# Performance work log

Hardware: AMD Instinct MI355X
Metric: run time of the kernel (lower is better)

Reference implementation:

```python
import jax, jax.numpy as jnp
import numpy as np

N = 100000      # nodes
E = 1600000     # edges (self-loops added in reference, as PyG GATConv does)
DIN = 512
DOUT = 16
H = 8           # heads (both layers)
C1 = 8          # out_channels of gat1
NEG_SLOPE = 0.2


def setup_inputs() -> dict:
    key = jax.random.key(0)
    ks = jax.random.split(key, 12)
    s = 0.05  # small init scale
    return {
        "x": jax.random.normal(ks[0], (N, DIN), jnp.float32),
        "edge_index": jax.random.randint(ks[1], (2, E), 0, N, jnp.int32),
        "W1": jax.random.normal(ks[2], (DIN, H * C1), jnp.float32) * s,
        "att_src1": jax.random.normal(ks[3], (H, C1), jnp.float32) * s,
        "att_dst1": jax.random.normal(ks[4], (H, C1), jnp.float32) * s,
        "bias1": jnp.zeros((H * C1,), jnp.float32),
        "prelu_w": jnp.float32(0.25),
        "W2": jax.random.normal(ks[5], (H * C1, H * DOUT), jnp.float32) * s,
        "att_src2": jax.random.normal(ks[6], (H, DOUT), jnp.float32) * s,
        "att_dst2": jax.random.normal(ks[7], (H, DOUT), jnp.float32) * s,
        "bias2": jnp.zeros((DOUT,), jnp.float32),
    }


def gat_layer(x, src, dst, W, a_src, a_dst, bias, heads, outc, concat):
    """PyG-style GATConv (eval mode, self-loops already in src/dst)."""
    n = x.shape[0]
    h = (x @ W).reshape(n, heads, outc)                 # [N, H, C]
    alpha_s = jnp.sum(h * a_src, axis=-1)               # [N, H]
    alpha_d = jnp.sum(h * a_dst, axis=-1)               # [N, H]
    # per-edge score, softmax grouped by destination node
    e = jax.nn.leaky_relu(alpha_s[src] + alpha_d[dst], NEG_SLOPE)   # [E', H]
    emax = jax.ops.segment_max(e, dst, num_segments=n)              # [N, H]
    ex = jnp.exp(e - emax[dst])
    denom = jax.ops.segment_sum(ex, dst, num_segments=n)            # [N, H]
    alpha = ex / denom[dst]                                         # [E', H]
    # weighted aggregation of source features
    out = jax.ops.segment_sum(h[src] * alpha[..., None], dst, num_segments=n)  # [N, H, C]
    out = out.reshape(n, heads * outc) if concat else out.mean(axis=1)
    return out + bias


def reference(x, edge_index, W1, att_src1, att_dst1, bias1, prelu_w,
              W2, att_src2, att_dst2, bias2):
    # add self-loops (PyG GATConv default add_self_loops=True)
    loops = jnp.arange(N, dtype=edge_index.dtype)
    src = jnp.concatenate([edge_index[0], loops])
    dst = jnp.concatenate([edge_index[1], loops])

    h = gat_layer(x, src, dst, W1, att_src1, att_dst1, bias1, H, C1, True)   # [N, 64]
    h = jnp.where(h >= 0, h, prelu_w * h)                                    # PReLU
    h = gat_layer(h, src, dst, W2, att_src2, att_dst2, bias2, H, DOUT, False)  # [N, DOUT]
    return jax.nn.log_softmax(h, axis=1)
```

## Files before the change

### kernel.cpp

```cpp
#include <hip/hip_runtime.h>
#include <hip/hip_bf16.h>

#define NN 100000
#define EE 1600000
#define ET (EE + NN)
#define NBK 391
#define NBLK 208
#define STAGE_CAP 5120

typedef unsigned short ushort_t;
typedef short short8 __attribute__((ext_vector_type(8)));
typedef float f32x4 __attribute__((ext_vector_type(4)));

static __device__ __forceinline__ float b2f(unsigned short u) {
    return __uint_as_float(((unsigned int)u) << 16);
}
static __device__ __forceinline__ unsigned short f2b(float f) {
    unsigned int x = __float_as_uint(f);
    return (unsigned short)((x + 0x7fffu + ((x >> 16) & 1u)) >> 16);
}

__global__ __launch_bounds__(256) void ktrans(const float* __restrict__ W1,
                                              const float* __restrict__ W2,
                                              ushort_t* __restrict__ W1T,
                                              ushort_t* __restrict__ W2T) {
    int tid = blockIdx.x * 256 + threadIdx.x;
    if (tid < 32768) {
        int k = tid >> 6, c = tid & 63;
        W1T[c * 512 + k] = f2b(W1[tid]);
    } else if (tid < 40960) {
        int t = tid - 32768;
        int k = t >> 7, c = t & 127;
        W2T[c * 64 + k] = f2b(W2[t]);
    }
}

__global__ __launch_bounds__(256) void kgemm1(const float* __restrict__ x,
                                              const ushort_t* __restrict__ w1t,
                                              ushort_t* __restrict__ h1) {
    __shared__ __align__(16) ushort_t xs[64][136];
    const int tid = threadIdx.x;
    const int wid = tid >> 6, lane = tid & 63;
    const int l15 = lane & 15, qq = lane >> 4;
    const int row0 = blockIdx.x * 64;
    f32x4 acc[4];
#pragma unroll
    for (int i = 0; i < 4; ++i) acc[i] = (f32x4)0.f;
    for (int kc = 0; kc < 4; ++kc) {
        float4 f[8];
#pragma unroll
        for (int i = 0; i < 8; ++i) {
            int f4i = tid + 256 * i;
            int rr = f4i >> 5;
            int cc = f4i & 31;
            long gr = (long)min(row0 + rr, NN - 1);
            f[i] = *(const float4*)(x + gr * 512 + kc * 128 + cc * 4);
        }
        __syncthreads();
#pragma unroll
        for (int i = 0; i < 8; ++i) {
            int f4i = tid + 256 * i;
            int rr = f4i >> 5, cc = f4i & 31;
            uint2 uu;
            uu.x = ((unsigned)f2b(f[i].y) << 16) | f2b(f[i].x);
            uu.y = ((unsigned)f2b(f[i].w) << 16) | f2b(f[i].z);
            *(uint2*)&xs[rr][cc * 4] = uu;
        }
        __syncthreads();
#pragma unroll
        for (int ks = 0; ks < 4; ++ks) {
            short8 b = *(const short8*)(w1t + (size_t)(wid * 16 + l15) * 512 + kc * 128 + ks * 32 + qq * 8);
#pragma unroll
            for (int mt = 0; mt < 4; ++mt) {
                short8 a = *(const short8*)&xs[mt * 16 + l15][ks * 32 + qq * 8];
                acc[mt] = __builtin_amdgcn_mfma_f32_16x16x32_bf16(a, b, acc[mt], 0, 0, 0);
            }
        }
    }
#pragma unroll
    for (int mt = 0; mt < 4; ++mt) {
        int node = row0 + mt * 16 + qq * 4;
#pragma unroll
        for (int rr = 0; rr < 4; ++rr) {
            if (node + rr < NN)
                h1[(size_t)(node + rr) * 64 + wid * 16 + l15] = f2b(acc[mt][rr]);
        }
    }
}

__global__ __launch_bounds__(256) void kgemm2(const ushort_t* __restrict__ hin,
                                              const ushort_t* __restrict__ w2t,
                                              ushort_t* __restrict__ h2) {
    __shared__ __align__(16) ushort_t xs[64][72];
    const int tid = threadIdx.x;
    const int wid = tid >> 6, lane = tid & 63;
    const int l15 = lane & 15, qq = lane >> 4;
    const int row0 = blockIdx.x * 64;
    const int r = tid >> 2, seg = tid & 3;
    const long grow = (long)min(row0 + r, NN - 1);
    const uint4* gp = (const uint4*)(hin + grow * 64 + seg * 16);
    uint4 v0 = gp[0], v1 = gp[1];
    uint4* lp = (uint4*)&xs[r][seg * 16];
    lp[0] = v0; lp[1] = v1;
    __syncthreads();
    f32x4 acc[4][2];
#pragma unroll
    for (int i = 0; i < 4; ++i)
#pragma unroll
        for (int j = 0; j < 2; ++j) acc[i][j] = (f32x4)0.f;
#pragma unroll
    for (int ks = 0; ks < 2; ++ks) {
        short8 a[4];
#pragma unroll
        for (int mt = 0; mt < 4; ++mt)
            a[mt] = *(const short8*)&xs[mt * 16 + l15][ks * 32 + qq * 8];
#pragma unroll
        for (int nt = 0; nt < 2; ++nt) {
            short8 b = *(const short8*)(w2t + (size_t)(wid * 32 + nt * 16 + l15) * 64 + ks * 32 + qq * 8);
#pragma unroll
            for (int mt = 0; mt < 4; ++mt)
                acc[mt][nt] = __builtin_amdgcn_mfma_f32_16x16x32_bf16(a[mt], b, acc[mt][nt], 0, 0, 0);
        }
    }
#pragma unroll
    for (int mt = 0; mt < 4; ++mt) {
        int node = row0 + mt * 16 + qq * 4;
#pragma unroll
        for (int nt = 0; nt < 2; ++nt) {
            int col = wid * 32 + nt * 16 + l15;
#pragma unroll
            for (int rr = 0; rr < 4; ++rr) {
                if (node + rr < NN)
                    h2[(size_t)(node + rr) * 128 + col] = f2b(acc[mt][nt][rr]);
            }
        }
    }
}


__global__ __launch_bounds__(256) void kbinh(const int* __restrict__ ei,
                                             int* __restrict__ bbcnt) {
    __shared__ int hist[NBK];
    const int t = threadIdx.x, blk = blockIdx.x;
    for (int i = t; i < NBK; i += 256) hist[i] = 0;
    __syncthreads();
    const int e0 = blk * 8192;
#pragma unroll
    for (int i = 0; i < 32; ++i) {
        int e = e0 + t + 256 * i;
        if (e < ET) {
            int dst = (e < EE) ? ei[EE + e] : (e - EE);
            atomicAdd(&hist[dst >> 8], 1);
        }
    }
    __syncthreads();
    for (int i = t; i < NBK; i += 256) bbcnt[blk * NBK + i] = hist[i];
}

__global__ __launch_bounds__(512) void kbscan(int* __restrict__ bbcnt,
                                              int* __restrict__ bbase) {
    __shared__ int tot[512];
    const int t = threadIdx.x;
    int total = 0;
    if (t < NBK) {
        int run = 0;
#pragma unroll 4
        for (int blk = 0; blk < NBLK; ++blk) {
            int idx = blk * NBK + t;
            int v = bbcnt[idx];
            bbcnt[idx] = run;
            run += v;
        }
        total = run;
    }
    tot[t] = total;
    __syncthreads();
    for (int off = 1; off < 512; off <<= 1) {
        int u = (t >= off) ? tot[t - off] : 0;
        __syncthreads();
        tot[t] += u;
        __syncthreads();
    }
    if (t < NBK) bbase[t] = tot[t] - total;
    if (t == 0) bbase[NBK] = ET;
}

__global__ __launch_bounds__(256) void kbinsct(const int* __restrict__ ei,
                                               const int* __restrict__ bbcnt,
                                               const int* __restrict__ bbase,
                                               unsigned* __restrict__ pairs) {
    __shared__ int cur[NBK];
    const int t = threadIdx.x, blk = blockIdx.x;
    for (int i = t; i < NBK; i += 256) cur[i] = bbase[i] + bbcnt[blk * NBK + i];
    __syncthreads();
    const int e0 = blk * 8192;
#pragma unroll
    for (int i = 0; i < 32; ++i) {
        int e = e0 + t + 256 * i;
        if (e < ET) {
            int src, dst;
            if (e < EE) { src = ei[e]; dst = ei[EE + e]; } else { src = dst = e - EE; }
            int pos = atomicAdd(&cur[dst >> 8], 1);
            pairs[pos] = (unsigned)src | ((unsigned)(dst & 255) << 17);
        }
    }
}

__global__ __launch_bounds__(256) void kscat2(const int* __restrict__ bbase,
                                              const unsigned* __restrict__ pairs,
                                              int* __restrict__ rowp,
                                              int* __restrict__ srt) {
    __shared__ int hist[256];
    __shared__ int scn[256];
    __shared__ int cur[256];
    __shared__ unsigned stage[STAGE_CAP];
    const int t = threadIdx.x, b = blockIdx.x;
    const int j0 = bbase[b], j1 = bbase[b + 1];
    const int cnt = j1 - j0;
    hist[t] = 0;
    __syncthreads();
    for (int i = t; i < cnt; i += 256) {
        unsigned p = pairs[j0 + i];
        if (i < STAGE_CAP) stage[i] = p;
        atomicAdd(&hist[p >> 17], 1);
    }
    __syncthreads();
    const int h = hist[t];
    scn[t] = h;
    __syncthreads();
    for (int off = 1; off < 256; off <<= 1) {
        int u = (t >= off) ? scn[t - off] : 0;
        __syncthreads();
        scn[t] += u;
        __syncthreads();
    }
    const int pref = scn[t] - h;
    const int node = b * 256 + t;
    if (node < NN) rowp[node] = j0 + pref;
    if (b == 0 && t == 0) rowp[NN] = ET;
    cur[t] = pref;
    __syncthreads();
    for (int i = t; i < cnt; i += 256) {
        unsigned p = (i < STAGE_CAP) ? stage[i] : pairs[j0 + i];
        int l = (int)(p >> 17);
        int pos = atomicAdd(&cur[l], 1);
        srt[j0 + pos] = (int)(p & 0x1FFFFu);
    }
}

__global__ __launch_bounds__(256) void kagg1(const int* __restrict__ rowp,
                                             const int* __restrict__ srt,
                                             const ushort_t* __restrict__ h1,
                                             const float* __restrict__ aws,
                                             const float* __restrict__ awd,
                                             const float* __restrict__ b1,
                                             const float* __restrict__ pw,
                                             ushort_t* __restrict__ hin) {
    int tid = blockIdx.x * 256 + threadIdx.x;
    int n = tid >> 4;
    int sub = tid & 15;
    int h = sub >> 1, half = sub & 1;
    float as_w[8], ad_w[8];
#pragma unroll
    for (int c = 0; c < 8; ++c) { as_w[c] = aws[h * 8 + c]; ad_w[c] = awd[h * 8 + c]; }
    uint4 hd = *(const uint4*)(h1 + (size_t)n * 64 + h * 8);
    const ushort_t* hdp = (const ushort_t*)&hd;
    float ad = 0.f;
#pragma unroll
    for (int c = 0; c < 8; ++c) ad += b2f(hdp[c]) * ad_w[c];
    int j0 = rowp[n], j1 = rowp[n + 1];
    float num[8]; float den = 0.f;
#pragma unroll
    for (int c = 0; c < 8; ++c) num[c] = 0.f;
    int j = j0 + half;
    uint4 hv;
    if (j < j1) {
        int s = srt[j];
        hv = *(const uint4*)(h1 + (size_t)s * 64 + h * 8);
    }
    while (j < j1) {
        int jn = j + 2;
        uint4 hn;
        if (jn < j1) {
            int sn = srt[jn];
            hn = *(const uint4*)(h1 + (size_t)sn * 64 + h * 8);
        }
        const ushort_t* hp = (const ushort_t*)&hv;
        float va[8];
#pragma unroll
        for (int c = 0; c < 8; ++c) va[c] = b2f(hp[c]);
        float sc = ad;
#pragma unroll
        for (int c = 0; c < 8; ++c) sc += va[c] * as_w[c];
        sc = (sc >= 0.f) ? sc : 0.2f * sc;
        float w = __expf(sc);
        den += w;
#pragma unroll
        for (int c = 0; c < 8; ++c) num[c] += w * va[c];
        j = jn;
        hv = hn;
    }
#pragma unroll
    for (int c = 0; c < 8; ++c) num[c] += __shfl_xor(num[c], 1);
    den += __shfl_xor(den, 1);
    if (half == 0) {
        float inv = 1.f / den;
        float pwf = pw[0];
        ushort_t o[8];
#pragma unroll
        for (int c = 0; c < 8; ++c) {
            float v = num[c] * inv + b1[h * 8 + c];
            v = (v >= 0.f) ? v : pwf * v;
            o[c] = f2b(v);
        }
        *(uint4*)(hin + (size_t)n * 64 + h * 8) = *(uint4*)o;
    }
}

__global__ __launch_bounds__(256) void kagg2(const int* __restrict__ rowp,
                                             const int* __restrict__ srt,
                                             const ushort_t* __restrict__ h2,
                                             const float* __restrict__ aws,
                                             const float* __restrict__ awd,
                                             const float* __restrict__ b2,
                                             float* __restrict__ out) {
    __shared__ float red[16][17];
    int t = threadIdx.x;
    int nl = t >> 4, sub = t & 15;
    int h = sub >> 1, half = sub & 1;
    int n = blockIdx.x * 16 + nl;
    for (int i = t; i < 16 * 17; i += 256) ((float*)red)[i] = 0.f;
    __syncthreads();
    float as_w[16], ad_w[16];
#pragma unroll
    for (int c = 0; c < 16; ++c) { as_w[c] = aws[h * 16 + c]; ad_w[c] = awd[h * 16 + c]; }
    uint4 d0 = *(const uint4*)(h2 + (size_t)n * 128 + h * 16);
    uint4 d1 = *(const uint4*)(h2 + (size_t)n * 128 + h * 16 + 8);
    const ushort_t* dp0 = (const ushort_t*)&d0;
    const ushort_t* dp1 = (const ushort_t*)&d1;
    float ad = 0.f;
#pragma unroll
    for (int c = 0; c < 8; ++c) { ad += b2f(dp0[c]) * ad_w[c]; ad += b2f(dp1[c]) * ad_w[8 + c]; }
    int j0 = rowp[n], j1 = rowp[n + 1];
    float num[16]; float den = 0.f;
#pragma unroll
    for (int c = 0; c < 16; ++c) num[c] = 0.f;
    int j = j0 + half;
    uint4 v0, v1;
    if (j < j1) {
        int s = srt[j];
        const uint4* rp = (const uint4*)(h2 + (size_t)s * 128 + h * 16);
        v0 = rp[0]; v1 = rp[1];
    }
    while (j < j1) {
        int jn = j + 2;
        uint4 n0, n1;
        if (jn < j1) {
            int sn = srt[jn];
            const uint4* rp = (const uint4*)(h2 + (size_t)sn * 128 + h * 16);
            n0 = rp[0]; n1 = rp[1];
        }
        const ushort_t* p0 = (const ushort_t*)&v0;
        const ushort_t* p1 = (const ushort_t*)&v1;
        float va[16];
#pragma unroll
        for (int c = 0; c < 8; ++c) { va[c] = b2f(p0[c]); va[8 + c] = b2f(p1[c]); }
        float sc = ad;
#pragma unroll
        for (int c = 0; c < 16; ++c) sc += va[c] * as_w[c];
        sc = (sc >= 0.f) ? sc : 0.2f * sc;
        float w = __expf(sc);
        den += w;
#pragma unroll
        for (int c = 0; c < 16; ++c) num[c] += w * va[c];
        j = jn;
        v0 = n0; v1 = n1;
    }
#pragma unroll
    for (int c = 0; c < 16; ++c) num[c] += __shfl_xor(num[c], 1);
    den += __shfl_xor(den, 1);
    float sden = 0.125f / den;
#pragma unroll
    for (int k = 0; k < 8; ++k) {
        int c = half * 8 + ((h + k) & 7);
        atomicAdd(&red[nl][c], num[c] * sden);
    }
    __syncthreads();
    if (t < 16) {
        float v[16];
#pragma unroll
        for (int d = 0; d < 16; ++d) v[d] = red[t][d] + b2[d];
        float m = v[0];
#pragma unroll
        for (int d = 1; d < 16; ++d) m = fmaxf(m, v[d]);
        float sum = 0.f;
#pragma unroll
        for (int d = 0; d < 16; ++d) sum += __expf(v[d] - m);
        float ls = __logf(sum) + m;
        float* op = out + (size_t)(blockIdx.x * 16 + t) * 16;
#pragma unroll
        for (int d = 0; d < 16; ++d) op[d] = v[d] - ls;
    }
}

extern "C" void kernel_launch(void* const* d_in, const int* in_sizes, int n_in,
                              void* d_out, int out_size, void* d_ws, size_t ws_size,
                              hipStream_t stream) {
    const float* x    = (const float*)d_in[0];
    const int*   ei   = (const int*)d_in[1];
    const float* W1   = (const float*)d_in[2];
    const float* aws1 = (const float*)d_in[3];
    const float* awd1 = (const float*)d_in[4];
    const float* b1   = (const float*)d_in[5];
    const float* pw   = (const float*)d_in[6];
    const float* W2   = (const float*)d_in[7];
    const float* aws2 = (const float*)d_in[8];
    const float* awd2 = (const float*)d_in[9];
    const float* b2   = (const float*)d_in[10];
    float* out = (float*)d_out;

    char* ws = (char*)d_ws;
    int*      srt   = (int*)(ws + 0);
    int*      rowp  = (int*)(ws + 6800000);
    int*      bbcnt = (int*)(ws + 7200256);
    int*      bbase = (int*)(ws + 7600384);
    unsigned* pairs = (unsigned*)(ws + 8000000);
    ushort_t* hin   = (ushort_t*)(ws + 8000000);
    ushort_t* h1    = (ushort_t*)(ws + 20800000);
    ushort_t* h2    = (ushort_t*)(ws + 20800000);
    ushort_t* W1T   = (ushort_t*)(ws + 46400000);
    ushort_t* W2T   = (ushort_t*)(ws + 46465536);

    ktrans<<<160, 256, 0, stream>>>(W1, W2, W1T, W2T);
    kgemm1<<<1563, 256, 0, stream>>>(x, W1T, h1);
    kbinh<<<NBLK, 256, 0, stream>>>(ei, bbcnt);
    kbscan<<<1, 512, 0, stream>>>(bbcnt, bbase);
    kbinsct<<<NBLK, 256, 0, stream>>>(ei, bbcnt, bbase, pairs);
    kscat2<<<NBK, 256, 0, stream>>>(bbase, pairs, rowp, srt);
    kagg1<<<6250, 256, 0, stream>>>(rowp, srt, h1, aws1, awd1, b1, pw, hin);
    kgemm2<<<1563, 256, 0, stream>>>(hin, W2T, h2);
    kagg2<<<6250, 256, 0, stream>>>(rowp, srt, h2, aws2, awd2, b2, out);
}
```

Baseline: 575.4 us.

## Co-schedule CSR build with GEMM1 and precompute per-node attention scores

Merges the weight transpose with the destination histogram and splits the first GEMM across the two CSR scatter kernels. Independent work now shares launches and can fill idle CUs during the small scatter grids. Adds kalpha1/kalpha2 kernels that compute per-node source and destination attention logits once, so the aggregation loops read a scalar per edge instead of recomputing a dot product per edge. Shrinks the staging buffer so the fused kernel's shared memory stays smaller. The cost is extra launches, extra global traffic for the logit arrays, and a scattered 4-byte load per edge.

```diff
diff --git a/kernel.cpp b/kernel.cpp
--- a/kernel.cpp
+++ b/kernel.cpp
@@ -6,7 +6,7 @@
 #define ET (EE + NN)
 #define NBK 391
 #define NBLK 208
-#define STAGE_CAP 5120
+#define STAGE_CAP 4096
 
 typedef unsigned short ushort_t;
 typedef short short8 __attribute__((ext_vector_type(8)));
@@ -20,29 +20,13 @@
     return (unsigned short)((x + 0x7fffu + ((x >> 16) & 1u)) >> 16);
 }
 
-__global__ __launch_bounds__(256) void ktrans(const float* __restrict__ W1,
-                                              const float* __restrict__ W2,
-                                              ushort_t* __restrict__ W1T,
-                                              ushort_t* __restrict__ W2T) {
-    int tid = blockIdx.x * 256 + threadIdx.x;
-    if (tid < 32768) {
-        int k = tid >> 6, c = tid & 63;
-        W1T[c * 512 + k] = f2b(W1[tid]);
-    } else if (tid < 40960) {
-        int t = tid - 32768;
-        int k = t >> 7, c = t & 127;
-        W2T[c * 64 + k] = f2b(W2[t]);
-    }
-}
-
-__global__ __launch_bounds__(256) void kgemm1(const float* __restrict__ x,
-                                              const ushort_t* __restrict__ w1t,
-                                              ushort_t* __restrict__ h1) {
-    __shared__ __align__(16) ushort_t xs[64][136];
-    const int tid = threadIdx.x;
+static __device__ void gemm1_body(const float* __restrict__ x,
+                                  const ushort_t* __restrict__ w1t,
+                                  ushort_t* __restrict__ h1,
+                                  char* smem_, int row0, int tid) {
+    ushort_t (*xs)[136] = (ushort_t (*)[136])smem_;
     const int wid = tid >> 6, lane = tid & 63;
     const int l15 = lane & 15, qq = lane >> 4;
-    const int row0 = blockIdx.x * 64;
     f32x4 acc[4];
 #pragma unroll
     for (int i = 0; i < 4; ++i) acc[i] = (f32x4)0.f;
@@ -85,6 +69,255 @@
             if (node + rr < NN)
                 h1[(size_t)(node + rr) * 64 + wid * 16 + l15] = f2b(acc[mt][rr]);
         }
+    }
+}
+
+__global__ __launch_bounds__(256) void kfuse0(const float* __restrict__ W1,
+                                              const float* __restrict__ W2,
+                                              ushort_t* __restrict__ W1T,
+                                              ushort_t* __restrict__ W2T,
+                                              const int* __restrict__ ei,
+                                              int* __restrict__ bbcnt) {
+    __shared__ int hist[NBK];
+    const int t = threadIdx.x;
+    if ((int)blockIdx.x < 160) {
+        int tid = blockIdx.x * 256 + t;
+        if (tid < 32768) {
+            int k = tid >> 6, c = tid & 63;
+            W1T[c * 512 + k] = f2b(W1[tid]);
+        } else if (tid < 40960) {
+            int q = tid - 32768;
+            int k = q >> 7, c = q & 127;
+            W2T[c * 64 + k] = f2b(W2[q]);
+        }
+    } else {
+        const int blk = blockIdx.x - 160;
+        for (int i = t; i < NBK; i += 256) hist[i] = 0;
+        __syncthreads();
+        const int e0 = blk * 8192;
+#pragma unroll
+        for (int i = 0; i < 32; ++i) {
+            int e = e0 + t + 256 * i;
+            if (e < ET) {
+                int dst = (e < EE) ? ei[EE + e] : (e - EE);
+                atomicAdd(&hist[dst >> 8], 1);
+            }
+        }
+        __syncthreads();
+        for (int i = t; i < NBK; i += 256) bbcnt[blk * NBK + i] = hist[i];
+    }
+}
+
+__global__ __launch_bounds__(512) void kbscan(int* __restrict__ bbcnt,
+                                              int* __restrict__ bbase) {
+    __shared__ int tot[512];
+    const int t = threadIdx.x;
+    int total = 0;
+    if (t < NBK) {
+        int run = 0;
+#pragma unroll 8
+        for (int blk = 0; blk < NBLK; ++blk) {
+            int idx = blk * NBK + t;
+            int v = bbcnt[idx];
+            bbcnt[idx] = run;
+            run += v;
+        }
+        total = run;
+    }
+    tot[t] = total;
+    __syncthreads();
+    for (int off = 1; off < 512; off <<= 1) {
+        int u = (t >= off) ? tot[t - off] : 0;
+        __syncthreads();
+        tot[t] += u;
+        __syncthreads();
+    }
+    if (t < NBK) bbase[t] = tot[t] - total;
+    if (t == 0) bbase[NBK] = ET;
+}
+
+__global__ __launch_bounds__(256) void kfuse1(const int* __restrict__ ei,
+                                              const int* __restrict__ bbcnt,
+                                              const int* __restrict__ bbase,
+                                              unsigned* __restrict__ pairs,
+                                              const float* __restrict__ x,
+                                              const ushort_t* __restrict__ w1t,
+                                              ushort_t* __restrict__ h1) {
+    __shared__ __align__(16) char smem[17408];
+    const int t = threadIdx.x;
+    if ((int)blockIdx.x < NBLK) {
+        int* cur = (int*)smem;
+        const int blk = blockIdx.x;
+        for (int i = t; i < NBK; i += 256) cur[i] = bbase[i] + bbcnt[blk * NBK + i];
+        __syncthreads();
+        const int e0 = blk * 8192;
+#pragma unroll
+        for (int i = 0; i < 32; ++i) {
+            int e = e0 + t + 256 * i;
+            if (e < ET) {
+                int src, dst;
+                if (e < EE) { src = ei[e]; dst = ei[EE + e]; } else { src = dst = e - EE; }
+                int pos = atomicAdd(&cur[dst >> 8], 1);
+                pairs[pos] = (unsigned)src | ((unsigned)(dst & 255) << 17);
+            }
+        }
+    } else {
+        gemm1_body(x, w1t, h1, smem, (blockIdx.x - NBLK) * 64, t);
+    }
+}
+
+__global__ __launch_bounds__(256) void kfuse2(const int* __restrict__ bbase,
+                                              const unsigned* __restrict__ pairs,
+                                              int* __restrict__ rowp,
+                                              int* __restrict__ srt,
+                                              const float* __restrict__ x,
+                                              const ushort_t* __restrict__ w1t,
+                                              ushort_t* __restrict__ h1) {
+    __shared__ __align__(16) char smem[19456];
+    const int t = threadIdx.x;
+    if ((int)blockIdx.x < NBK) {
+        int* hist = (int*)smem;
+        int* scn = hist + 256;
+        int* cur = scn + 256;
+        unsigned* stage = (unsigned*)(smem + 3072);
+        const int b = blockIdx.x;
+        const int j0 = bbase[b], j1 = bbase[b + 1];
+        const int cnt = j1 - j0;
+        hist[t] = 0;
+        __syncthreads();
+        for (int i = t; i < cnt; i += 256) {
+            unsigned p = pairs[j0 + i];
+            if (i < STAGE_CAP) stage[i] = p;
+            atomicAdd(&hist[p >> 17], 1);
+        }
+        __syncthreads();
+        const int h = hist[t];
+        scn[t] = h;
+        __syncthreads();
+        for (int off = 1; off < 256; off <<= 1) {
+            int u = (t >= off) ? scn[t - off] : 0;
+            __syncthreads();
+            scn[t] += u;
+            __syncthreads();
+        }
+        const int pref = scn[t] - h;
+        const int node = b * 256 + t;
+        if (node < NN) rowp[node] = j0 + pref;
+        if (b == 0 && t == 0) rowp[NN] = ET;
+        cur[t] = pref;
+        __syncthreads();
+        for (int i = t; i < cnt; i += 256) {
+            unsigned p = (i < STAGE_CAP) ? stage[i] : pairs[j0 + i];
+            int l = (int)(p >> 17);
+            int pos = atomicAdd(&cur[l], 1);
+            srt[j0 + pos] = (int)(p & 0x1FFFFu);
+        }
+    } else {
+        gemm1_body(x, w1t, h1, smem, (782 + (int)blockIdx.x - NBK) * 64, t);
+    }
+}
+
+__global__ __launch_bounds__(256) void kalpha1(const ushort_t* __restrict__ h1,
+                                               const float* __restrict__ aws,
+                                               const float* __restrict__ awd,
+                                               float* __restrict__ a1s,
+                                               float* __restrict__ a1d) {
+    int tid = blockIdx.x * 256 + threadIdx.x;
+    int n = tid >> 3, h = tid & 7;
+    uint4 v = *(const uint4*)(h1 + (size_t)n * 64 + h * 8);
+    const ushort_t* p = (const ushort_t*)&v;
+    float s = 0.f, d = 0.f;
+#pragma unroll
+    for (int c = 0; c < 8; ++c) {
+        float f = b2f(p[c]);
+        s += f * aws[h * 8 + c];
+        d += f * awd[h * 8 + c];
+    }
+    a1s[tid] = s;
+    a1d[tid] = d;
+}
+
+__global__ __launch_bounds__(256) void kalpha2(const ushort_t* __restrict__ h2,
+                                               const float* __restrict__ aws,
+                                               const float* __restrict__ awd,
+                                               float* __restrict__ a2s,
+                                               float* __restrict__ a2d) {
+    int tid = blockIdx.x * 256 + threadIdx.x;
+    int n = tid >> 3, h = tid & 7;
+    uint4 v0 = *(const uint4*)(h2 + (size_t)n * 128 + h * 16);
+    uint4 v1 = *(const uint4*)(h2 + (size_t)n * 128 + h * 16 + 8);
+    const ushort_t* p0 = (const ushort_t*)&v0;
+    const ushort_t* p1 = (const ushort_t*)&v1;
+    float s = 0.f, d = 0.f;
+#pragma unroll
+    for (int c = 0; c < 8; ++c) {
+        float fa = b2f(p0[c]), fb = b2f(p1[c]);
+        s += fa * aws[h * 16 + c];
+        d += fa * awd[h * 16 + c];
+        s += fb * aws[h * 16 + 8 + c];
+        d += fb * awd[h * 16 + 8 + c];
+    }
+    a2s[tid] = s;
+    a2d[tid] = d;
+}
+
+__global__ __launch_bounds__(256) void kagg1(const int* __restrict__ rowp,
+                                             const int* __restrict__ srt,
+                                             const ushort_t* __restrict__ h1,
+                                             const float* __restrict__ a1s,
+                                             const float* __restrict__ a1d,
+                                             const float* __restrict__ b1,
+                                             const float* __restrict__ pw,
+                                             ushort_t* __restrict__ hin) {
+    int tid = blockIdx.x * 256 + threadIdx.x;
+    int n = tid >> 4;
+    int sub = tid & 15;
+    int h = sub >> 1, half = sub & 1;
+    float ad = a1d[n * 8 + h];
+    int j0 = rowp[n], j1 = rowp[n + 1];
+    float num[8]; float den = 0.f;
+#pragma unroll
+    for (int c = 0; c < 8; ++c) num[c] = 0.f;
+    int j = j0 + half;
+    uint4 hv; float al = 0.f;
+    if (j < j1) {
+        int s = srt[j];
+        al = a1s[s * 8 + h];
+        hv = *(const uint4*)(h1 + (size_t)s * 64 + h * 8);
+    }
+    while (j < j1) {
+        int jn = j + 2;
+        uint4 hn; float aln = 0.f;
+        if (jn < j1) {
+            int sn = srt[jn];
+            aln = a1s[sn * 8 + h];
+            hn = *(const uint4*)(h1 + (size_t)sn * 64 + h * 8);
+        }
+        float sc = al + ad;
+        sc = (sc >= 0.f) ? sc : 0.2f * sc;
+        float w = __expf(sc);
+        den += w;
+        const ushort_t* hp = (const ushort_t*)&hv;
+#pragma unroll
+        for (int c = 0; c < 8; ++c) num[c] += w * b2f(hp[c]);
+        j = jn;
+        hv = hn;
+        al = aln;
+    }
+#pragma unroll
+    for (int c = 0; c < 8; ++c) num[c] += __shfl_xor(num[c], 1);
+    den += __shfl_xor(den, 1);
+    if (half == 0) {
+        float inv = 1.f / den;
+        float pwf = pw[0];
+        ushort_t o[8];
+#pragma unroll
+        for (int c = 0; c < 8; ++c) {
+            float v = num[c] * inv + b1[h * 8 + c];
+            v = (v >= 0.f) ? v : pwf * v;
+            o[c] = f2b(v);
+        }
+        *(uint4*)(hin + (size_t)n * 64 + h * 8) = *(uint4*)o;
     }
 }
 
@@ -137,191 +370,11 @@
     }
 }
 
-
-__global__ __launch_bounds__(256) void kbinh(const int* __restrict__ ei,
-                                             int* __restrict__ bbcnt) {
-    __shared__ int hist[NBK];
-    const int t = threadIdx.x, blk = blockIdx.x;
-    for (int i = t; i < NBK; i += 256) hist[i] = 0;
-    __syncthreads();
-    const int e0 = blk * 8192;
-#pragma unroll
-    for (int i = 0; i < 32; ++i) {
-        int e = e0 + t + 256 * i;
-        if (e < ET) {
-            int dst = (e < EE) ? ei[EE + e] : (e - EE);
-            atomicAdd(&hist[dst >> 8], 1);
-        }
-    }
-    __syncthreads();
-    for (int i = t; i < NBK; i += 256) bbcnt[blk * NBK + i] = hist[i];
-}
-
-__global__ __launch_bounds__(512) void kbscan(int* __restrict__ bbcnt,
-                                              int* __restrict__ bbase) {
-    __shared__ int tot[512];
-    const int t = threadIdx.x;
-    int total = 0;
-    if (t < NBK) {
-        int run = 0;
-#pragma unroll 4
-        for (int blk = 0; blk < NBLK; ++blk) {
-            int idx = blk * NBK + t;
-            int v = bbcnt[idx];
-            bbcnt[idx] = run;
-            run += v;
-        }
-        total = run;
-    }
-    tot[t] = total;
-    __syncthreads();
-    for (int off = 1; off < 512; off <<= 1) {
-        int u = (t >= off) ? tot[t - off] : 0;
-        __syncthreads();
-        tot[t] += u;
-        __syncthreads();
-    }
-    if (t < NBK) bbase[t] = tot[t] - total;
-    if (t == 0) bbase[NBK] = ET;
-}
-
-__global__ __launch_bounds__(256) void kbinsct(const int* __restrict__ ei,
-                                               const int* __restrict__ bbcnt,
-                                               const int* __restrict__ bbase,
-                                               unsigned* __restrict__ pairs) {
-    __shared__ int cur[NBK];
-    const int t = threadIdx.x, blk = blockIdx.x;
-    for (int i = t; i < NBK; i += 256) cur[i] = bbase[i] + bbcnt[blk * NBK + i];
-    __syncthreads();
-    const int e0 = blk * 8192;
-#pragma unroll
-    for (int i = 0; i < 32; ++i) {
-        int e = e0 + t + 256 * i;
-        if (e < ET) {
-            int src, dst;
-            if (e < EE) { src = ei[e]; dst = ei[EE + e]; } else { src = dst = e - EE; }
-            int pos = atomicAdd(&cur[dst >> 8], 1);
-            pairs[pos] = (unsigned)src | ((unsigned)(dst & 255) << 17);
-        }
-    }
-}
-
-__global__ __launch_bounds__(256) void kscat2(const int* __restrict__ bbase,
-                                              const unsigned* __restrict__ pairs,
-                                              int* __restrict__ rowp,
-                                              int* __restrict__ srt) {
-    __shared__ int hist[256];
-    __shared__ int scn[256];
-    __shared__ int cur[256];
-    __shared__ unsigned stage[STAGE_CAP];
-    const int t = threadIdx.x, b = blockIdx.x;
-    const int j0 = bbase[b], j1 = bbase[b + 1];
-    const int cnt = j1 - j0;
-    hist[t] = 0;
-    __syncthreads();
-    for (int i = t; i < cnt; i += 256) {
-        unsigned p = pairs[j0 + i];
-        if (i < STAGE_CAP) stage[i] = p;
-        atomicAdd(&hist[p >> 17], 1);
-    }
-    __syncthreads();
-    const int h = hist[t];
-    scn[t] = h;
-    __syncthreads();
-    for (int off = 1; off < 256; off <<= 1) {
-        int u = (t >= off) ? scn[t - off] : 0;
-        __syncthreads();
-        scn[t] += u;
-        __syncthreads();
-    }
-    const int pref = scn[t] - h;
-    const int node = b * 256 + t;
-    if (node < NN) rowp[node] = j0 + pref;
-    if (b == 0 && t == 0) rowp[NN] = ET;
-    cur[t] = pref;
-    __syncthreads();
-    for (int i = t; i < cnt; i += 256) {
-        unsigned p = (i < STAGE_CAP) ? stage[i] : pairs[j0 + i];
-        int l = (int)(p >> 17);
-        int pos = atomicAdd(&cur[l], 1);
-        srt[j0 + pos] = (int)(p & 0x1FFFFu);
-    }
-}
-
-__global__ __launch_bounds__(256) void kagg1(const int* __restrict__ rowp,
-                                             const int* __restrict__ srt,
-                                             const ushort_t* __restrict__ h1,
-                                             const float* __restrict__ aws,
-                                             const float* __restrict__ awd,
-                                             const float* __restrict__ b1,
-                                             const float* __restrict__ pw,
-                                             ushort_t* __restrict__ hin) {
-    int tid = blockIdx.x * 256 + threadIdx.x;
-    int n = tid >> 4;
-    int sub = tid & 15;
-    int h = sub >> 1, half = sub & 1;
-    float as_w[8], ad_w[8];
-#pragma unroll
-    for (int c = 0; c < 8; ++c) { as_w[c] = aws[h * 8 + c]; ad_w[c] = awd[h * 8 + c]; }
-    uint4 hd = *(const uint4*)(h1 + (size_t)n * 64 + h * 8);
-    const ushort_t* hdp = (const ushort_t*)&hd;
-    float ad = 0.f;
-#pragma unroll
-    for (int c = 0; c < 8; ++c) ad += b2f(hdp[c]) * ad_w[c];
-    int j0 = rowp[n], j1 = rowp[n + 1];
-    float num[8]; float den = 0.f;
-#pragma unroll
-    for (int c = 0; c < 8; ++c) num[c] = 0.f;
-    int j = j0 + half;
-    uint4 hv;
-    if (j < j1) {
-        int s = srt[j];
-        hv = *(const uint4*)(h1 + (size_t)s * 64 + h * 8);
-    }
-    while (j < j1) {
-        int jn = j + 2;
-        uint4 hn;
-        if (jn < j1) {
-            int sn = srt[jn];
-            hn = *(const uint4*)(h1 + (size_t)sn * 64 + h * 8);
-        }
-        const ushort_t* hp = (const ushort_t*)&hv;
-        float va[8];
-#pragma unroll
-        for (int c = 0; c < 8; ++c) va[c] = b2f(hp[c]);
-        float sc = ad;
-#pragma unroll
-        for (int c = 0; c < 8; ++c) sc += va[c] * as_w[c];
-        sc = (sc >= 0.f) ? sc : 0.2f * sc;
-        float w = __expf(sc);
-        den += w;
-#pragma unroll
-        for (int c = 0; c < 8; ++c) num[c] += w * va[c];
-        j = jn;
-        hv = hn;
-    }
-#pragma unroll
-    for (int c = 0; c < 8; ++c) num[c] += __shfl_xor(num[c], 1);
-    den += __shfl_xor(den, 1);
-    if (half == 0) {
-        float inv = 1.f / den;
-        float pwf = pw[0];
-        ushort_t o[8];
-#pragma unroll
-        for (int c = 0; c < 8; ++c) {
-            float v = num[c] * inv + b1[h * 8 + c];
-            v = (v >= 0.f) ? v : pwf * v;
-            o[c] = f2b(v);
-        }
-        *(uint4*)(hin + (size_t)n * 64 + h * 8) = *(uint4*)o;
-    }
-}
-
 __global__ __launch_bounds__(256) void kagg2(const int* __restrict__ rowp,
                                              const int* __restrict__ srt,
                                              const ushort_t* __restrict__ h2,
-                                             const float* __restrict__ aws,
-                                             const float* __restrict__ awd,
+                                             const float* __restrict__ a2s,
+                                             const float* __restrict__ a2d,
                                              const float* __restrict__ b2,
                                              float* __restrict__ out) {
     __shared__ float red[16][17];
@@ -331,50 +384,42 @@
     int n = blockIdx.x * 16 + nl;
     for (int i = t; i < 16 * 17; i += 256) ((float*)red)[i] = 0.f;
     __syncthreads();
-    float as_w[16], ad_w[16];
-#pragma unroll
-    for (int c = 0; c < 16; ++c) { as_w[c] = aws[h * 16 + c]; ad_w[c] = awd[h * 16 + c]; }
-    uint4 d0 = *(const uint4*)(h2 + (size_t)n * 128 + h * 16);
-    uint4 d1 = *(const uint4*)(h2 + (size_t)n * 128 + h * 16 + 8);
-    const ushort_t* dp0 = (const ushort_t*)&d0;
-    const ushort_t* dp1 = (const ushort_t*)&d1;
-    float ad = 0.f;
-#pragma unroll
-    for (int c = 0; c < 8; ++c) { ad += b2f(dp0[c]) * ad_w[c]; ad += b2f(dp1[c]) * ad_w[8 + c]; }
+    float ad = a2d[n * 8 + h];
     int j0 = rowp[n], j1 = rowp[n + 1];
     float num[16]; float den = 0.f;
 #pragma unroll
     for (int c = 0; c < 16; ++c) num[c] = 0.f;
     int j = j0 + half;
-    uint4 v0, v1;
+    uint4 v0, v1; float al = 0.f;
     if (j < j1) {
         int s = srt[j];
+        al = a2s[s * 8 + h];
         const uint4* rp = (const uint4*)(h2 + (size_t)s * 128 + h * 16);
         v0 = rp[0]; v1 = rp[1];
     }
     while (j < j1) {
         int jn = j + 2;
-        uint4 n0, n1;
+        uint4 n0, n1; float aln = 0.f;
         if (jn < j1) {
             int sn = srt[jn];
+            aln = a2s[sn * 8 + h];
             const uint4* rp = (const uint4*)(h2 + (size_t)sn * 128 + h * 16);
             n0 = rp[0]; n1 = rp[1];
         }
-        const ushort_t* p0 = (const ushort_t*)&v0;
-        const ushort_t* p1 = (const ushort_t*)&v1;
-        float va[16];
-#pragma unroll
-        for (int c = 0; c < 8; ++c) { va[c] = b2f(p0[c]); va[8 + c] = b2f(p1[c]); }
-        float sc = ad;
-#pragma unroll
-        for (int c = 0; c < 16; ++c) sc += va[c] * as_w[c];
+        float sc = al + ad;
         sc = (sc >= 0.f) ? sc : 0.2f * sc;
         float w = __expf(sc);
         den += w;
-#pragma unroll
-        for (int c = 0; c < 16; ++c) num[c] += w * va[c];
+        const ushort_t* p0 = (const ushort_t*)&v0;
+        const ushort_t* p1 = (const ushort_t*)&v1;
+#pragma unroll
+        for (int c = 0; c < 8; ++c) {
+            num[c] += w * b2f(p0[c]);
+            num[8 + c] += w * b2f(p1[c]);
+        }
         j = jn;
         v0 = n0; v1 = n1;
+        al = aln;
     }
 #pragma unroll
     for (int c = 0; c < 16; ++c) num[c] += __shfl_xor(num[c], 1);
@@ -426,18 +471,22 @@
     int*      bbase = (int*)(ws + 7600384);
     unsigned* pairs = (unsigned*)(ws + 8000000);
     ushort_t* hin   = (ushort_t*)(ws + 8000000);
+    float*    a2s   = (float*)(ws + 8000000);
+    float*    a2d   = (float*)(ws + 11200000);
     ushort_t* h1    = (ushort_t*)(ws + 20800000);
     ushort_t* h2    = (ushort_t*)(ws + 20800000);
+    float*    a1s   = (float*)(ws + 33600000);
+    float*    a1d   = (float*)(ws + 36800000);
     ushort_t* W1T   = (ushort_t*)(ws + 46400000);
     ushort_t* W2T   = (ushort_t*)(ws + 46465536);
 
-    ktrans<<<160, 256, 0, stream>>>(W1, W2, W1T, W2T);
-    kgemm1<<<1563, 256, 0, stream>>>(x, W1T, h1);
-    kbinh<<<NBLK, 256, 0, stream>>>(ei, bbcnt);
+    kfuse0<<<160 + NBLK, 256, 0, stream>>>(W1, W2, W1T, W2T, ei, bbcnt);
     kbscan<<<1, 512, 0, stream>>>(bbcnt, bbase);
-    kbinsct<<<NBLK, 256, 0, stream>>>(ei, bbcnt, bbase, pairs);
-    kscat2<<<NBK, 256, 0, stream>>>(bbase, pairs, rowp, srt);
-    kagg1<<<6250, 256, 0, stream>>>(rowp, srt, h1, aws1, awd1, b1, pw, hin);
+    kfuse1<<<NBLK + 782, 256, 0, stream>>>(ei, bbcnt, bbase, pairs, x, W1T, h1);
+    kfuse2<<<NBK + 781, 256, 0, stream>>>(bbase, pairs, rowp, srt, x, W1T, h1);
+    kalpha1<<<3125, 256, 0, stream>>>(h1, aws1, awd1, a1s, a1d);
+    kagg1<<<6250, 256, 0, stream>>>(rowp, srt, h1, a1s, a1d, b1, pw, hin);
     kgemm2<<<1563, 256, 0, stream>>>(hin, W2T, h2);
-    kagg2<<<6250, 256, 0, stream>>>(rowp, srt, h2, aws2, awd2, b2, out);
-}
+    kalpha2<<<3125, 256, 0, stream>>>(h2, aws2, awd2, a2s, a2d);
+    kagg2<<<6250, 256, 0, stream>>>(rowp, srt, h2, a2s, a2d, b2, out);
+}
```

Measured after the change: 582.8 us. About the same (+1.3%).

## Co-schedule GEMM1 blocks with CSR build kernels and shuffle-reduce layer-2 output

Applied to the files above, without the earlier changes.

Merges the weight transpose with the destination histogram into one launch. The first GEMM is split into two halves that run as extra blocks inside the bin-scatter and local-sort kernels, so the memory-bound CSR construction overlaps with matrix compute and the separate launches go away. The second aggregation kernel now reduces heads with warp shuffles instead of shared-memory atomics and a barrier, and every lane writes one output. The staging capacity is reduced so the shared buffer fits the fused kernel, which sends more of the large buckets through the global-memory fallback.

```diff
diff --git a/kernel.cpp b/kernel.cpp
--- a/kernel.cpp
+++ b/kernel.cpp
@@ -6,7 +6,7 @@
 #define ET (EE + NN)
 #define NBK 391
 #define NBLK 208
-#define STAGE_CAP 5120
+#define STAGE_CAP 4096
 
 typedef unsigned short ushort_t;
 typedef short short8 __attribute__((ext_vector_type(8)));
@@ -20,29 +20,13 @@
     return (unsigned short)((x + 0x7fffu + ((x >> 16) & 1u)) >> 16);
 }
 
-__global__ __launch_bounds__(256) void ktrans(const float* __restrict__ W1,
-                                              const float* __restrict__ W2,
-                                              ushort_t* __restrict__ W1T,
-                                              ushort_t* __restrict__ W2T) {
-    int tid = blockIdx.x * 256 + threadIdx.x;
-    if (tid < 32768) {
-        int k = tid >> 6, c = tid & 63;
-        W1T[c * 512 + k] = f2b(W1[tid]);
-    } else if (tid < 40960) {
-        int t = tid - 32768;
-        int k = t >> 7, c = t & 127;
-        W2T[c * 64 + k] = f2b(W2[t]);
-    }
-}
-
-__global__ __launch_bounds__(256) void kgemm1(const float* __restrict__ x,
-                                              const ushort_t* __restrict__ w1t,
-                                              ushort_t* __restrict__ h1) {
-    __shared__ __align__(16) ushort_t xs[64][136];
-    const int tid = threadIdx.x;
+static __device__ void gemm1_body(const float* __restrict__ x,
+                                  const ushort_t* __restrict__ w1t,
+                                  ushort_t* __restrict__ h1,
+                                  char* smem_, int row0, int tid) {
+    ushort_t (*xs)[136] = (ushort_t (*)[136])smem_;
     const int wid = tid >> 6, lane = tid & 63;
     const int l15 = lane & 15, qq = lane >> 4;
-    const int row0 = blockIdx.x * 64;
     f32x4 acc[4];
 #pragma unroll
     for (int i = 0; i < 4; ++i) acc[i] = (f32x4)0.f;
@@ -85,6 +69,220 @@
             if (node + rr < NN)
                 h1[(size_t)(node + rr) * 64 + wid * 16 + l15] = f2b(acc[mt][rr]);
         }
+    }
+}
+
+__global__ __launch_bounds__(256) void kfuse0(const float* __restrict__ W1,
+                                              const float* __restrict__ W2,
+                                              ushort_t* __restrict__ W1T,
+                                              ushort_t* __restrict__ W2T,
+                                              const int* __restrict__ ei,
+                                              int* __restrict__ bbcnt) {
+    __shared__ int hist[NBK];
+    const int t = threadIdx.x;
+    if ((int)blockIdx.x < 160) {
+        int tid = blockIdx.x * 256 + t;
+        if (tid < 32768) {
+            int k = tid >> 6, c = tid & 63;
+            W1T[c * 512 + k] = f2b(W1[tid]);
+        } else if (tid < 40960) {
+            int q = tid - 32768;
+            int k = q >> 7, c = q & 127;
+            W2T[c * 64 + k] = f2b(W2[q]);
+        }
+    } else {
+        const int blk = blockIdx.x - 160;
+        for (int i = t; i < NBK; i += 256) hist[i] = 0;
+        __syncthreads();
+        const int e0 = blk * 8192;
+#pragma unroll
+        for (int i = 0; i < 32; ++i) {
+            int e = e0 + t + 256 * i;
+            if (e < ET) {
+                int dst = (e < EE) ? ei[EE + e] : (e - EE);
+                atomicAdd(&hist[dst >> 8], 1);
+            }
+        }
+        __syncthreads();
+        for (int i = t; i < NBK; i += 256) bbcnt[blk * NBK + i] = hist[i];
+    }
+}
+
+__global__ __launch_bounds__(512) void kbscan(int* __restrict__ bbcnt,
+                                              int* __restrict__ bbase) {
+    __shared__ int tot[512];
+    const int t = threadIdx.x;
+    int total = 0;
+    if (t < NBK) {
+        int run = 0;
+#pragma unroll 8
+        for (int blk = 0; blk < NBLK; ++blk) {
+            int idx = blk * NBK + t;
+            int v = bbcnt[idx];
+            bbcnt[idx] = run;
+            run += v;
+        }
+        total = run;
+    }
+    tot[t] = total;
+    __syncthreads();
+    for (int off = 1; off < 512; off <<= 1) {
+        int u = (t >= off) ? tot[t - off] : 0;
+        __syncthreads();
+        tot[t] += u;
+        __syncthreads();
+    }
+    if (t < NBK) bbase[t] = tot[t] - total;
+    if (t == 0) bbase[NBK] = ET;
+}
+
+__global__ __launch_bounds__(256) void kfuse1(const int* __restrict__ ei,
+                                              const int* __restrict__ bbcnt,
+                                              const int* __restrict__ bbase,
+                                              unsigned* __restrict__ pairs,
+                                              const float* __restrict__ x,
+                                              const ushort_t* __restrict__ w1t,
+                                              ushort_t* __restrict__ h1) {
+    __shared__ __align__(16) char smem[17408];
+    const int t = threadIdx.x;
+    if ((int)blockIdx.x < NBLK) {
+        int* cur = (int*)smem;
+        const int blk = blockIdx.x;
+        for (int i = t; i < NBK; i += 256) cur[i] = bbase[i] + bbcnt[blk * NBK + i];
+        __syncthreads();
+        const int e0 = blk * 8192;
+#pragma unroll
+        for (int i = 0; i < 32; ++i) {
+            int e = e0 + t + 256 * i;
+            if (e < ET) {
+                int src, dst;
+                if (e < EE) { src = ei[e]; dst = ei[EE + e]; } else { src = dst = e - EE; }
+                int pos = atomicAdd(&cur[dst >> 8], 1);
+                pairs[pos] = (unsigned)src | ((unsigned)(dst & 255) << 17);
+            }
+        }
+    } else {
+        gemm1_body(x, w1t, h1, smem, (blockIdx.x - NBLK) * 64, t);
+    }
+}
+
+__global__ __launch_bounds__(256) void kfuse2(const int* __restrict__ bbase,
+                                              const unsigned* __restrict__ pairs,
+                                              int* __restrict__ rowp,
+                                              int* __restrict__ srt,
+                                              const float* __restrict__ x,
+                                              const ushort_t* __restrict__ w1t,
+                                              ushort_t* __restrict__ h1) {
+    __shared__ __align__(16) char smem[19456];
+    const int t = threadIdx.x;
+    if ((int)blockIdx.x < NBK) {
+        int* hist = (int*)smem;
+        int* scn = hist + 256;
+        int* cur = scn + 256;
+        unsigned* stage = (unsigned*)(smem + 3072);
+        const int b = blockIdx.x;
+        const int j0 = bbase[b], j1 = bbase[b + 1];
+        const int cnt = j1 - j0;
+        hist[t] = 0;
+        __syncthreads();
+        for (int i = t; i < cnt; i += 256) {
+            unsigned p = pairs[j0 + i];
+            if (i < STAGE_CAP) stage[i] = p;
+            atomicAdd(&hist[p >> 17], 1);
+        }
+        __syncthreads();
+        const int h = hist[t];
+        scn[t] = h;
+        __syncthreads();
+        for (int off = 1; off < 256; off <<= 1) {
+            int u = (t >= off) ? scn[t - off] : 0;
+            __syncthreads();
+            scn[t] += u;
+            __syncthreads();
+        }
+        const int pref = scn[t] - h;
+        const int node = b * 256 + t;
+        if (node < NN) rowp[node] = j0 + pref;
+        if (b == 0 && t == 0) rowp[NN] = ET;
+        cur[t] = pref;
+        __syncthreads();
+        for (int i = t; i < cnt; i += 256) {
+            unsigned p = (i < STAGE_CAP) ? stage[i] : pairs[j0 + i];
+            int l = (int)(p >> 17);
+            int pos = atomicAdd(&cur[l], 1);
+            srt[j0 + pos] = (int)(p & 0x1FFFFu);
+        }
+    } else {
+        gemm1_body(x, w1t, h1, smem, (782 + (int)blockIdx.x - NBK) * 64, t);
+    }
+}
+
+__global__ __launch_bounds__(256) void kagg1(const int* __restrict__ rowp,
+                                             const int* __restrict__ srt,
+                                             const ushort_t* __restrict__ h1,
+                                             const float* __restrict__ aws,
+                                             const float* __restrict__ awd,
+                                             const float* __restrict__ b1,
+                                             const float* __restrict__ pw,
+                                             ushort_t* __restrict__ hin) {
+    int tid = blockIdx.x * 256 + threadIdx.x;
+    int n = tid >> 4;
+    int sub = tid & 15;
+    int h = sub >> 1, half = sub & 1;
+    float as_w[8], ad_w[8];
+#pragma unroll
+    for (int c = 0; c < 8; ++c) { as_w[c] = aws[h * 8 + c]; ad_w[c] = awd[h * 8 + c]; }
+    uint4 hd = *(const uint4*)(h1 + (size_t)n * 64 + h * 8);
+    const ushort_t* hdp = (const ushort_t*)&hd;
+    float ad = 0.f;
+#pragma unroll
+    for (int c = 0; c < 8; ++c) ad += b2f(hdp[c]) * ad_w[c];
+    int j0 = rowp[n], j1 = rowp[n + 1];
+    float num[8]; float den = 0.f;
+#pragma unroll
+    for (int c = 0; c < 8; ++c) num[c] = 0.f;
+    int j = j0 + half;
+    uint4 hv;
+    if (j < j1) {
+        int s = srt[j];
+        hv = *(const uint4*)(h1 + (size_t)s * 64 + h * 8);
+    }
+    while (j < j1) {
+        int jn = j + 2;
+        uint4 hn;
+        if (jn < j1) {
+            int sn = srt[jn];
+            hn = *(const uint4*)(h1 + (size_t)sn * 64 + h * 8);
+        }
+        const ushort_t* hp = (const ushort_t*)&hv;
+        float va[8];
+#pragma unroll
+        for (int c = 0; c < 8; ++c) va[c] = b2f(hp[c]);
+        float sc = ad;
+#pragma unroll
+        for (int c = 0; c < 8; ++c) sc += va[c] * as_w[c];
+        sc = (sc >= 0.f) ? sc : 0.2f * sc;
+        float w = __expf(sc);
+        den += w;
+#pragma unroll
+        for (int c = 0; c < 8; ++c) num[c] += w * va[c];
+        j = jn;
+        hv = hn;
+    }
+#pragma unroll
+    for (int c = 0; c < 8; ++c) num[c] += __shfl_xor(num[c], 1);
+    den += __shfl_xor(den, 1);
+    if (half == 0) {
+        float inv = 1.f / den;
+        float pwf = pw[0];
+        ushort_t o[8];
+#pragma unroll
+        for (int c = 0; c < 8; ++c) {
+            float v = num[c] * inv + b1[h * 8 + c];
+            v = (v >= 0.f) ? v : pwf * v;
+            o[c] = f2b(v);
+        }
+        *(uint4*)(hin + (size_t)n * 64 + h * 8) = *(uint4*)o;
     }
 }
 
@@ -137,186 +335,6 @@
     }
 }
 
-
-__global__ __launch_bounds__(256) void kbinh(const int* __restrict__ ei,
-                                             int* __restrict__ bbcnt) {
-    __shared__ int hist[NBK];
-    const int t = threadIdx.x, blk = blockIdx.x;
-    for (int i = t; i < NBK; i += 256) hist[i] = 0;
-    __syncthreads();
-    const int e0 = blk * 8192;
-#pragma unroll
-    for (int i = 0; i < 32; ++i) {
-        int e = e0 + t + 256 * i;
-        if (e < ET) {
-            int dst = (e < EE) ? ei[EE + e] : (e - EE);
-            atomicAdd(&hist[dst >> 8], 1);
-        }
-    }
-    __syncthreads();
-    for (int i = t; i < NBK; i += 256) bbcnt[blk * NBK + i] = hist[i];
-}
-
-__global__ __launch_bounds__(512) void kbscan(int* __restrict__ bbcnt,
-                                              int* __restrict__ bbase) {
-    __shared__ int tot[512];
-    const int t = threadIdx.x;
-    int total = 0;
-    if (t < NBK) {
-        int run = 0;
-#pragma unroll 4
-        for (int blk = 0; blk < NBLK; ++blk) {
-            int idx = blk * NBK + t;
-            int v = bbcnt[idx];
-            bbcnt[idx] = run;
-            run += v;
-        }
-        total = run;
-    }
-    tot[t] = total;
-    __syncthreads();
-    for (int off = 1; off < 512; off <<= 1) {
-        int u = (t >= off) ? tot[t - off] : 0;
-        __syncthreads();
-        tot[t] += u;
-        __syncthreads();
-    }
-    if (t < NBK) bbase[t] = tot[t] - total;
-    if (t == 0) bbase[NBK] = ET;
-}
-
-__global__ __launch_bounds__(256) void kbinsct(const int* __restrict__ ei,
-                                               const int* __restrict__ bbcnt,
-                                               const int* __restrict__ bbase,
-                                               unsigned* __restrict__ pairs) {
-    __shared__ int cur[NBK];
-    const int t = threadIdx.x, blk = blockIdx.x;
-    for (int i = t; i < NBK; i += 256) cur[i] = bbase[i] + bbcnt[blk * NBK + i];
-    __syncthreads();
-    const int e0 = blk * 8192;
-#pragma unroll
-    for (int i = 0; i < 32; ++i) {
-        int e = e0 + t + 256 * i;
-        if (e < ET) {
-            int src, dst;
-            if (e < EE) { src = ei[e]; dst = ei[EE + e]; } else { src = dst = e - EE; }
-            int pos = atomicAdd(&cur[dst >> 8], 1);
-            pairs[pos] = (unsigned)src | ((unsigned)(dst & 255) << 17);
-        }
-    }
-}
-
-__global__ __launch_bounds__(256) void kscat2(const int* __restrict__ bbase,
-                                              const unsigned* __restrict__ pairs,
-                                              int* __restrict__ rowp,
-                                              int* __restrict__ srt) {
-    __shared__ int hist[256];
-    __shared__ int scn[256];
-    __shared__ int cur[256];
-    __shared__ unsigned stage[STAGE_CAP];
-    const int t = threadIdx.x, b = blockIdx.x;
-    const int j0 = bbase[b], j1 = bbase[b + 1];
-    const int cnt = j1 - j0;
-    hist[t] = 0;
-    __syncthreads();
-    for (int i = t; i < cnt; i += 256) {
-        unsigned p = pairs[j0 + i];
-        if (i < STAGE_CAP) stage[i] = p;
-        atomicAdd(&hist[p >> 17], 1);
-    }
-    __syncthreads();
-    const int h = hist[t];
-    scn[t] = h;
-    __syncthreads();
-    for (int off = 1; off < 256; off <<= 1) {
-        int u = (t >= off) ? scn[t - off] : 0;
-        __syncthreads();
-        scn[t] += u;
-        __syncthreads();
-    }
-    const int pref = scn[t] - h;
-    const int node = b * 256 + t;
-    if (node < NN) rowp[node] = j0 + pref;
-    if (b == 0 && t == 0) rowp[NN] = ET;
-    cur[t] = pref;
-    __syncthreads();
-    for (int i = t; i < cnt; i += 256) {
-        unsigned p = (i < STAGE_CAP) ? stage[i] : pairs[j0 + i];
-        int l = (int)(p >> 17);
-        int pos = atomicAdd(&cur[l], 1);
-        srt[j0 + pos] = (int)(p & 0x1FFFFu);
-    }
-}
-
-__global__ __launch_bounds__(256) void kagg1(const int* __restrict__ rowp,
-                                             const int* __restrict__ srt,
-                                             const ushort_t* __restrict__ h1,
-                                             const float* __restrict__ aws,
-                                             const float* __restrict__ awd,
-                                             const float* __restrict__ b1,
-                                             const float* __restrict__ pw,
-                                             ushort_t* __restrict__ hin) {
-    int tid = blockIdx.x * 256 + threadIdx.x;
-    int n = tid >> 4;
-    int sub = tid & 15;
-    int h = sub >> 1, half = sub & 1;
-    float as_w[8], ad_w[8];
-#pragma unroll
-    for (int c = 0; c < 8; ++c) { as_w[c] = aws[h * 8 + c]; ad_w[c] = awd[h * 8 + c]; }
-    uint4 hd = *(const uint4*)(h1 + (size_t)n * 64 + h * 8);
-    const ushort_t* hdp = (const ushort_t*)&hd;
-    float ad = 0.f;
-#pragma unroll
-    for (int c = 0; c < 8; ++c) ad += b2f(hdp[c]) * ad_w[c];
-    int j0 = rowp[n], j1 = rowp[n + 1];
-    float num[8]; float den = 0.f;
-#pragma unroll
-    for (int c = 0; c < 8; ++c) num[c] = 0.f;
-    int j = j0 + half;
-    uint4 hv;
-    if (j < j1) {
-        int s = srt[j];
-        hv = *(const uint4*)(h1 + (size_t)s * 64 + h * 8);
-    }
-    while (j < j1) {
-        int jn = j + 2;
-        uint4 hn;
-        if (jn < j1) {
-            int sn = srt[jn];
-            hn = *(const uint4*)(h1 + (size_t)sn * 64 + h * 8);
-        }
-        const ushort_t* hp = (const ushort_t*)&hv;
-        float va[8];
-#pragma unroll
-        for (int c = 0; c < 8; ++c) va[c] = b2f(hp[c]);
-        float sc = ad;
-#pragma unroll
-        for (int c = 0; c < 8; ++c) sc += va[c] * as_w[c];
-        sc = (sc >= 0.f) ? sc : 0.2f * sc;
-        float w = __expf(sc);
-        den += w;
-#pragma unroll
-        for (int c = 0; c < 8; ++c) num[c] += w * va[c];
-        j = jn;
-        hv = hn;
-    }
-#pragma unroll
-    for (int c = 0; c < 8; ++c) num[c] += __shfl_xor(num[c], 1);
-    den += __shfl_xor(den, 1);
-    if (half == 0) {
-        float inv = 1.f / den;
-        float pwf = pw[0];
-        ushort_t o[8];
-#pragma unroll
-        for (int c = 0; c < 8; ++c) {
-            float v = num[c] * inv + b1[h * 8 + c];
-            v = (v >= 0.f) ? v : pwf * v;
-            o[c] = f2b(v);
-        }
-        *(uint4*)(hin + (size_t)n * 64 + h * 8) = *(uint4*)o;
-    }
-}
-
 __global__ __launch_bounds__(256) void kagg2(const int* __restrict__ rowp,
                                              const int* __restrict__ srt,
                                              const ushort_t* __restrict__ h2,
@@ -324,13 +342,10 @@
                                              const float* __restrict__ awd,
                                              const float* __restrict__ b2,
                                              float* __restrict__ out) {
-    __shared__ float red[16][17];
-    int t = threadIdx.x;
-    int nl = t >> 4, sub = t & 15;
+    int tid = blockIdx.x * 256 + threadIdx.x;
+    int n = tid >> 4;
+    int sub = tid & 15;
     int h = sub >> 1, half = sub & 1;
-    int n = blockIdx.x * 16 + nl;
-    for (int i = t; i < 16 * 17; i += 256) ((float*)red)[i] = 0.f;
-    __syncthreads();
     float as_w[16], ad_w[16];
 #pragma unroll
     for (int c = 0; c < 16; ++c) { as_w[c] = aws[h * 16 + c]; ad_w[c] = awd[h * 16 + c]; }
@@ -380,27 +395,23 @@
     for (int c = 0; c < 16; ++c) num[c] += __shfl_xor(num[c], 1);
     den += __shfl_xor(den, 1);
     float sden = 0.125f / den;
-#pragma unroll
-    for (int k = 0; k < 8; ++k) {
-        int c = half * 8 + ((h + k) & 7);
-        atomicAdd(&red[nl][c], num[c] * sden);
-    }
-    __syncthreads();
-    if (t < 16) {
-        float v[16];
-#pragma unroll
-        for (int d = 0; d < 16; ++d) v[d] = red[t][d] + b2[d];
-        float m = v[0];
-#pragma unroll
-        for (int d = 1; d < 16; ++d) m = fmaxf(m, v[d]);
-        float sum = 0.f;
-#pragma unroll
-        for (int d = 0; d < 16; ++d) sum += __expf(v[d] - m);
-        float ls = __logf(sum) + m;
-        float* op = out + (size_t)(blockIdx.x * 16 + t) * 16;
-#pragma unroll
-        for (int d = 0; d < 16; ++d) op[d] = v[d] - ls;
-    }
+    float v[16];
+#pragma unroll
+    for (int c = 0; c < 16; ++c) v[c] = num[c] * sden;
+#pragma unroll
+    for (int mask = 2; mask <= 8; mask <<= 1)
+#pragma unroll
+        for (int c = 0; c < 16; ++c) v[c] += __shfl_xor(v[c], mask);
+#pragma unroll
+    for (int c = 0; c < 16; ++c) v[c] += b2[c];
+    float m = v[0];
+#pragma unroll
+    for (int c = 1; c < 16; ++c) m = fmaxf(m, v[c]);
+    float sum = 0.f;
+#pragma unroll
+    for (int c = 0; c < 16; ++c) sum += __expf(v[c] - m);
+    float ls = __logf(sum) + m;
+    out[(size_t)n * 16 + sub] = v[sub] - ls;
 }
 
 extern "C" void kernel_launch(void* const* d_in, const int* in_sizes, int n_in,
@@ -431,12 +442,10 @@
     ushort_t* W1T   = (ushort_t*)(ws + 46400000);
     ushort_t* W2T   = (ushort_t*)(ws + 46465536);
 
-    ktrans<<<160, 256, 0, stream>>>(W1, W2, W1T, W2T);
-    kgemm1<<<1563, 256, 0, stream>>>(x, W1T, h1);
-    kbinh<<<NBLK, 256, 0, stream>>>(ei, bbcnt);
+    kfuse0<<<160 + NBLK, 256, 0, stream>>>(W1, W2, W1T, W2T, ei, bbcnt);
     kbscan<<<1, 512, 0, stream>>>(bbcnt, bbase);
-    kbinsct<<<NBLK, 256, 0, stream>>>(ei, bbcnt, bbase, pairs);
-    kscat2<<<NBK, 256, 0, stream>>>(bbase, pairs, rowp, srt);
+    kfuse1<<<NBLK + 782, 256, 0, stream>>>(ei, bbcnt, bbase, pairs, x, W1T, h1);
+    kfuse2<<<NBK + 781, 256, 0, stream>>>(bbase, pairs, rowp, srt, x, W1T, h1);
     kagg1<<<6250, 256, 0, stream>>>(rowp, srt, h1, aws1, awd1, b1, pw, hin);
     kgemm2<<<1563, 256, 0, stream>>>(hin, W2T, h2);
     kagg2<<<6250, 256, 0, stream>>>(rowp, srt, h2, aws2, awd2, b2, out);
```

Measured after the change: 502.5 us. 12.7% less time.
